# Optimization experiments

Measured on AMD Instinct MI355X. Metric: run time of the kernel, lower is better.

Reference implementation:

```python
import jax, jax.numpy as jnp
import numpy as np

EPS = 1e-12  # F.normalize eps


def _l2norm(v):
    n = jnp.sqrt(jnp.sum(v * v, axis=-1, keepdims=True))
    return v / jnp.maximum(n, EPS)


def setup_inputs() -> dict:
    key = jax.random.key(0)
    ks = jax.random.split(key, 6)
    B, S, D, F, E = 2, 2048, 1024, 4096, 8
    std = 0.02
    return {
        "x": jax.random.normal(ks[0], (B, S, D), jnp.float32),
        "Wp": jax.random.normal(ks[1], (D, D), jnp.float32) * (1.0 / np.sqrt(D)),
        "sim_matrix": jax.random.normal(ks[2], (E, D), jnp.float32) * std,
        "temperature": jnp.asarray(1.0, jnp.float32),
        "W1": jax.random.normal(ks[3], (E, D, F), jnp.float32) * (1.0 / np.sqrt(D)),
        "b1": jnp.zeros((E, F), jnp.float32),
        "W2": jax.random.normal(ks[4], (E, F, D), jnp.float32) * (1.0 / np.sqrt(F)),
        "b2": jnp.zeros((E, D), jnp.float32),
    }


def reference(x, Wp, sim_matrix, temperature, W1, b1, W2, b2):
    # ---- cosine gate ----
    E = sim_matrix.shape[0]
    top_k = 2
    proj = jnp.einsum("bsd,ed->bse", x, Wp)            # Linear(d,d), weight [out,in]
    pn = _l2norm(proj)                                   # [B,S,D]
    sn = _l2norm(sim_matrix)                             # [E,D]
    gate_scores = jnp.einsum("bsd,ed->bse", pn, sn) / temperature
    top_v, top_i = jax.lax.top_k(gate_scores, top_k)     # [B,S,K]
    gate_probs = jax.nn.softmax(top_v, axis=-1)          # [B,S,K]
    # per-token combine weight per expert: sum_k prob_k * 1[idx_k==e]
    comb = jnp.sum(jax.nn.one_hot(top_i, E, dtype=x.dtype) * gate_probs[..., None], axis=-2)  # [B,S,E]
    # ---- experts (dense over all experts, masked combine = original math) ----
    h = jax.nn.gelu(jnp.einsum("bsd,edf->ebsf", x, W1) + b1[:, None, None, :], approximate=False)
    eo = jnp.einsum("ebsf,efd->ebsd", h, W2) + b2[:, None, None, :]  # [E,B,S,D]
    out = jnp.einsum("ebsd,bse->bsd", eo, comb)
    return out
```

## Files before the change

### kernel.cpp

```cpp
#include <hip/hip_runtime.h>
#include <hip/hip_bf16.h>
#include <math.h>

#define NTOK 4096
#define DD 1024
#define FF 4096
#define NEXP 8
#define EBM 128
#define EBN 128
#define EBK 32
#define PAIR_CAP 9216
#define TILES_MAX 72

typedef short bf16x8 __attribute__((ext_vector_type(8)));
typedef float f32x4 __attribute__((ext_vector_type(4)));
typedef unsigned short u16x8 __attribute__((ext_vector_type(8)));

__device__ __forceinline__ ushort f2bf(float x) {
  unsigned u = __float_as_uint(x);
  unsigned r = (u + 0x7FFFu + ((u >> 16) & 1u)) >> 16;
  return (ushort)r;
}

__device__ __forceinline__ void async16(const void* g, void* l) {
  __builtin_amdgcn_global_load_lds(
      (const __attribute__((address_space(1))) char*)g,
      (__attribute__((address_space(3))) char*)l, 16, 0, 0);
}


__global__ void k_convert4(const float4* __restrict__ s, ushort* __restrict__ d, int n4) {
  int i = blockIdx.x * 256 + threadIdx.x;
  if (i >= n4) return;
  float4 v = s[i];
  ushort4 o;
  o.x = f2bf(v.x); o.y = f2bf(v.y); o.z = f2bf(v.z); o.w = f2bf(v.w);
  *(ushort4*)(d + (size_t)i * 4) = o;
}

__global__ void k_transpose(const float* __restrict__ src, ushort* __restrict__ dst,
                            int R, int C) {
  __shared__ float tile[128][65];
  int e = blockIdx.z;
  const float* s = src + (size_t)e * R * C;
  ushort* d = dst + (size_t)e * R * C;
  int c0 = blockIdx.x * 64, r0 = blockIdx.y * 128;
  int tid = threadIdx.x;
  int rr0 = tid >> 4;
  int cc4 = (tid & 15) * 4;
#pragma unroll
  for (int ps = 0; ps < 8; ++ps) {
    int r = ps * 16 + rr0;
    float4 v = *(const float4*)&s[(size_t)(r0 + r) * C + c0 + cc4];
    tile[r][cc4 + 0] = v.x; tile[r][cc4 + 1] = v.y;
    tile[r][cc4 + 2] = v.z; tile[r][cc4 + 3] = v.w;
  }
  __syncthreads();
  int cw = tid >> 4;
  int rp = (tid & 15) * 8;
#pragma unroll
  for (int pass = 0; pass < 4; ++pass) {
    int c = pass * 16 + cw;
    u16x8 o;
#pragma unroll
    for (int k = 0; k < 8; ++k) o[k] = f2bf(tile[rp + k][c]);
    *(u16x8*)&d[(size_t)(c0 + c) * R + r0 + rp] = o;
  }
}

__global__ void k_simnorm(const float* __restrict__ sim, double* __restrict__ snorm) {
  int wid = threadIdx.x >> 6, lane = threadIdx.x & 63;
  double s = 0.0;
  for (int d = lane; d < DD; d += 64) { double v = sim[wid * DD + d]; s += v * v; }
#pragma unroll
  for (int m = 32; m; m >>= 1) s += __shfl_down(s, m);
  if (lane == 0) snorm[wid] = sqrt(s);
}

__global__ void k_u(const float* __restrict__ wp, const float* __restrict__ sim,
                    const double* __restrict__ snorm, double* __restrict__ u) {
  int d = blockIdx.x * 256 + threadIdx.x;
  int e = blockIdx.y;
  double acc = 0.0;
#pragma unroll 8
  for (int o = 0; o < DD; ++o)
    acc += (double)wp[(size_t)o * DD + d] * (double)sim[e * DD + o];
  u[e * DD + d] = acc / fmax(snorm[e], 1e-12);
}

__global__ void k_nured(const float* __restrict__ part, float* __restrict__ nu) {
  int t = blockIdx.x * 256 + threadIdx.x;
  float s = 0.f;
#pragma unroll
  for (int i = 0; i < 16; ++i) s += part[t * 16 + i];
  nu[t] = s;
}

__global__ void k_gate(const float* __restrict__ x, const double* __restrict__ u,
                       const float* __restrict__ nu, const float* __restrict__ temp,
                       int* __restrict__ t2e, float* __restrict__ t2p) {
  int wid = threadIdx.x >> 6, lane = threadIdx.x & 63;
  int t = blockIdx.x * 4 + wid;
  double acc[NEXP];
#pragma unroll
  for (int e = 0; e < NEXP; ++e) acc[e] = 0.0;
  for (int d = lane; d < DD; d += 64) {
    double xv = x[(size_t)t * DD + d];
#pragma unroll
    for (int e = 0; e < NEXP; ++e) acc[e] += xv * u[e * DD + d];
  }
#pragma unroll
  for (int e = 0; e < NEXP; ++e)
    for (int m = 32; m; m >>= 1) acc[e] += __shfl_down(acc[e], m);
  if (lane == 0) {
    double den = fmax(sqrt((double)nu[t]), 1e-12) * (double)temp[0];
    double s[NEXP];
#pragma unroll
    for (int e = 0; e < NEXP; ++e) s[e] = acc[e] / den;
    int e1 = 0; double v1 = s[0];
    for (int e = 1; e < NEXP; ++e) if (s[e] > v1) { v1 = s[e]; e1 = e; }
    int e2 = -1; double v2 = -1e300;
    for (int e = 0; e < NEXP; ++e) if (e != e1 && s[e] > v2) { v2 = s[e]; e2 = e; }
    double z = exp(v2 - v1);
    double inv = 1.0 / (1.0 + z);
    t2e[t * 2] = e1; t2e[t * 2 + 1] = e2;
    t2p[t * 2] = (float)inv; t2p[t * 2 + 1] = (float)(z * inv);
  }
}

__global__ void k_count(const int* __restrict__ t2e, int* __restrict__ meta,
                        int* __restrict__ ptok, float* __restrict__ pp) {
  __shared__ int cnt[NEXP];
  int tid = threadIdx.x;
  if (tid < NEXP) cnt[tid] = 0;
  __syncthreads();
  for (int i = tid; i < NTOK * 2; i += 256) atomicAdd(&cnt[t2e[i]], 1);
  __syncthreads();
  if (tid == 0) {
    int off = 0;
    for (int e = 0; e < NEXP; ++e) {
      meta[e] = cnt[e];
      meta[8 + e] = off;
      off += ((cnt[e] + EBM - 1) / EBM) * EBM;
    }
    meta[16] = off;
    meta[17] = off / EBM;
    for (int e = 0; e < NEXP; ++e) meta[18 + e] = 0;
    int ti = 0;
    for (int e = 0; e < NEXP; ++e) {
      int nt = (cnt[e] + EBM - 1) / EBM;
      for (int k = 0; k < nt; ++k) meta[26 + ti++] = e;
    }
  }
  for (int i = tid; i < PAIR_CAP; i += 256) { ptok[i] = 0; pp[i] = 0.f; }
}

__global__ void k_scatter(const int* __restrict__ t2e, const float* __restrict__ t2p,
                          int* __restrict__ meta, int* __restrict__ ptok,
                          float* __restrict__ pp) {
  int i = blockIdx.x * 256 + threadIdx.x;
  if (i >= NTOK * 2) return;
  int e = t2e[i];
  int slot = atomicAdd(&meta[18 + e], 1);
  int pos = meta[8 + e] + slot;
  ptok[pos] = i >> 1;
  pp[pos] = t2p[i];
}

template <int EPI>
__launch_bounds__(256, 4)
__global__ void gemm_x(const ushort* __restrict__ Abase, const ushort* __restrict__ Bbase,
                       int K, int Brows,
                       const int* __restrict__ pair_tok, const float* __restrict__ pair_p,
                       const int* __restrict__ meta, const float* __restrict__ bias,
                       float* __restrict__ nu_part, ushort* __restrict__ hout,
                       float* __restrict__ outp, int g_tiles, int nby, int tile0) {
  __shared__ ushort As[2][EBM * EBK];
  __shared__ ushort Bs[2][EBN * EBK];
  __shared__ int tok_s[EBM];
  __shared__ float p_s[EBM];

  const int tid = threadIdx.x;
  const int lane = tid & 63;
  const int wid = tid >> 6;

  int tile, nb;
  {
    int bid = blockIdx.x;
    if ((g_tiles & 1) == 0 && (nby & 3) == 0) {
      int x = bid & 7, b = bid >> 3;
      int i = x >> 2, j = x & 3;
      int nt = g_tiles >> 1, np = nby >> 2;
      int t_loc = b / np, p_loc = b - t_loc * np;
      tile = i * nt + t_loc;
      nb = j * np + p_loc;
    } else {
      tile = bid % g_tiles;
      nb = bid / g_tiles;
    }
  }
  tile += tile0;

  int expert = 0;
  if constexpr (EPI != 0) {
    if (tile >= meta[17]) return;
    expert = meta[26 + tile];
    if (tid < EBM) {
      int pr = tile * EBM + tid;
      tok_s[tid] = pair_tok[pr];
      p_s[tid] = pair_p[pr];
    }
    __syncthreads();
  }

  const char* Ac = (const char*)Abase;
  const char* Bc = (const char*)(Bbase + (size_t)expert * Brows * K);

  const char* asrc[2];
  const char* bsrc[2];
#pragma unroll
  for (int i = 0; i < 2; ++i) {
    int c = i * 256 + tid;
    int m = c >> 2, cc = c & 3;
    int sw = (cc ^ (m & 3)) << 4;
    int arow;
    if constexpr (EPI == 1) arow = tok_s[m];
    else if constexpr (EPI == 2) arow = (tile - tile0) * EBM + m;
    else arow = tile * EBM + m;
    asrc[i] = Ac + (size_t)arow * K * 2 + sw;
    bsrc[i] = Bc + (size_t)(nb * EBN + m) * K * 2 + sw;
  }

  const int wr = wid >> 1, wc = wid & 1;
  const int l15 = lane & 15, lg = lane >> 4;

  f32x4 acc[4][4];
#pragma unroll
  for (int a = 0; a < 4; ++a)
#pragma unroll
    for (int b = 0; b < 4; ++b) acc[a][b] = (f32x4){0.f, 0.f, 0.f, 0.f};

  const int nk = K / EBK;

#pragma unroll
  for (int i = 0; i < 2; ++i) {
    async16(asrc[i], (char*)(&As[0][0]) + (i * 256 + wid * 64) * 16);
    async16(bsrc[i], (char*)(&Bs[0][0]) + (i * 256 + wid * 64) * 16);
  }

  for (int kt = 0; kt < nk; ++kt) {
    const int cur = kt & 1;
    __syncthreads();
    if (kt + 1 < nk) {
      const size_t ko = (size_t)(kt + 1) * EBK * 2;
#pragma unroll
      for (int i = 0; i < 2; ++i) {
        async16(asrc[i] + ko, (char*)(&As[cur ^ 1][0]) + (i * 256 + wid * 64) * 16);
        async16(bsrc[i] + ko, (char*)(&Bs[cur ^ 1][0]) + (i * 256 + wid * 64) * 16);
      }
    }
    const char* Ab = (const char*)(&As[cur][0]);
    const char* Bb = (const char*)(&Bs[cur][0]);
    bf16x8 af[4], bfr[4];
#pragma unroll
    for (int fi = 0; fi < 4; ++fi) {
      int r = wr * 64 + fi * 16 + l15;
      int cidx = lg ^ (r & 3);
      af[fi] = *(const bf16x8*)(Ab + r * 64 + cidx * 16);
    }
#pragma unroll
    for (int fj = 0; fj < 4; ++fj) {
      int r = wc * 64 + fj * 16 + l15;
      int cidx = lg ^ (r & 3);
      bfr[fj] = *(const bf16x8*)(Bb + r * 64 + cidx * 16);
    }
#pragma unroll
    for (int fi = 0; fi < 4; ++fi)
#pragma unroll
      for (int fj = 0; fj < 4; ++fj)
        acc[fi][fj] =
            __builtin_amdgcn_mfma_f32_16x16x32_bf16(af[fi], bfr[fj], acc[fi][fj], 0, 0, 0);
  }

  if constexpr (EPI == 0) {
#pragma unroll
    for (int fi = 0; fi < 4; ++fi) {
#pragma unroll
      for (int j = 0; j < 4; ++j) {
        float s = 0.f;
#pragma unroll
        for (int fj = 0; fj < 4; ++fj) { float v = acc[fi][fj][j]; s += v * v; }
        s += __shfl_xor(s, 1); s += __shfl_xor(s, 2);
        s += __shfl_xor(s, 4); s += __shfl_xor(s, 8);
        if (l15 == 0) {
          int row = tile * EBM + wr * 64 + fi * 16 + lg * 4 + j;
          nu_part[row * 16 + nb * 2 + wc] = s;
        }
      }
    }
  } else if constexpr (EPI == 1) {
    float bv[4];
#pragma unroll
    for (int fj = 0; fj < 4; ++fj)
      bv[fj] = bias[expert * FF + nb * EBN + wc * 64 + fj * 16 + l15];
#pragma unroll
    for (int fi = 0; fi < 4; ++fi)
#pragma unroll
      for (int fj = 0; fj < 4; ++fj)
#pragma unroll
        for (int j = 0; j < 4; ++j) {
          float v = acc[fi][fj][j] + bv[fj];
          float g = 0.5f * v * (1.0f + erff(v * 0.70710678118654752f));
          int rl = wr * 64 + fi * 16 + lg * 4 + j;
          size_t grow = (size_t)(tile - tile0) * EBM + rl;
          int col = nb * EBN + wc * 64 + fj * 16 + l15;
          hout[grow * FF + col] = f2bf(g);
        }
  } else {
    float bv[4];
#pragma unroll
    for (int fj = 0; fj < 4; ++fj)
      bv[fj] = bias[expert * DD + nb * EBN + wc * 64 + fj * 16 + l15];
#pragma unroll
    for (int fi = 0; fi < 4; ++fi) {
      int rl = wr * 64 + fi * 16 + lg * 4;
#pragma unroll
      for (int j = 0; j < 4; ++j) {
        int tok = tok_s[rl + j];
        float p = p_s[rl + j];
#pragma unroll
        for (int fj = 0; fj < 4; ++fj) {
          float v = (acc[fi][fj][j] + bv[fj]) * p;
          int col = nb * EBN + wc * 64 + fj * 16 + l15;
          atomicAdd(outp + (size_t)tok * DD + col, v);
        }
      }
    }
  }
}


extern "C" void kernel_launch(void* const* d_in, const int* in_sizes, int n_in,
                              void* d_out, int out_size, void* d_ws, size_t ws_size,
                              hipStream_t stream) {
  const float* x = (const float*)d_in[0];
  const float* wp = (const float*)d_in[1];
  const float* sim = (const float*)d_in[2];
  const float* temp = (const float*)d_in[3];
  const float* w1 = (const float*)d_in[4];
  const float* b1 = (const float*)d_in[5];
  const float* w2 = (const float*)d_in[6];
  const float* b2 = (const float*)d_in[7];
  float* out = (float*)d_out;

  char* w = (char*)d_ws;
  size_t off = 0;
  auto alloc = [&](size_t sz) {
    char* p = w + off;
    off = (off + sz + 255) & ~(size_t)255;
    return p;
  };
  double* u = (double*)alloc((size_t)NEXP * DD * 8);
  double* snorm = (double*)alloc(NEXP * 8);
  float* nu_part = (float*)alloc((size_t)NTOK * 16 * 4);
  float* nu = (float*)alloc((size_t)NTOK * 4);
  int* t2e = (int*)alloc((size_t)NTOK * 2 * 4);
  float* t2p = (float*)alloc((size_t)NTOK * 2 * 4);
  int* meta = (int*)alloc(512);
  int* ptok = (int*)alloc((size_t)PAIR_CAP * 4);
  float* pp = (float*)alloc((size_t)PAIR_CAP * 4);
  ushort* xbf = (ushort*)alloc((size_t)NTOK * DD * 2);
  ushort* wpbf = (ushort*)alloc((size_t)DD * DD * 2);
  ushort* w1t = (ushort*)alloc((size_t)NEXP * DD * FF * 2);
  ushort* w2t = (ushort*)alloc((size_t)NEXP * DD * FF * 2);
  size_t havail = (ws_size > off) ? (ws_size - off) : 0;
  int G = (int)(havail / ((size_t)EBM * FF * 2));
  if (G > TILES_MAX) G = TILES_MAX;
  if (G >= 8) G &= ~7;
  if (G < 1) G = 1;
  ushort* h = (ushort*)(w + off);

  hipMemsetAsync(d_out, 0, (size_t)out_size * 4, stream);

  k_convert4<<<dim3(NTOK * DD / 4 / 256), 256, 0, stream>>>((const float4*)x, xbf, NTOK * DD / 4);
  k_convert4<<<dim3(DD * DD / 4 / 256), 256, 0, stream>>>((const float4*)wp, wpbf, DD * DD / 4);
  k_transpose<<<dim3(FF / 64, DD / 128, NEXP), 256, 0, stream>>>(w1, w1t, DD, FF);
  k_transpose<<<dim3(DD / 64, FF / 128, NEXP), 256, 0, stream>>>(w2, w2t, FF, DD);
  k_simnorm<<<1, 512, 0, stream>>>(sim, snorm);
  k_u<<<dim3(DD / 256, NEXP), 256, 0, stream>>>(wp, sim, snorm, u);
  gemm_x<0><<<dim3((NTOK / EBM) * (DD / EBN)), 256, 0, stream>>>(
      xbf, wpbf, DD, DD, nullptr, nullptr, nullptr, nullptr, nu_part, nullptr, nullptr,
      NTOK / EBM, DD / EBN, 0);
  k_nured<<<dim3(NTOK / 256), 256, 0, stream>>>(nu_part, nu);
  k_gate<<<dim3(NTOK / 4), 256, 0, stream>>>(x, u, nu, temp, t2e, t2p);
  k_count<<<1, 256, 0, stream>>>(t2e, meta, ptok, pp);
  k_scatter<<<dim3(NTOK * 2 / 256), 256, 0, stream>>>(t2e, t2p, meta, ptok, pp);

  for (int t0 = 0; t0 < TILES_MAX; t0 += G) {
    int g = TILES_MAX - t0;
    if (g > G) g = G;
    gemm_x<1><<<dim3(g * (FF / EBN)), 256, 0, stream>>>(
        xbf, w1t, DD, FF, ptok, pp, meta, b1, nullptr, h, nullptr, g, FF / EBN, t0);
    gemm_x<2><<<dim3(g * (DD / EBN)), 256, 0, stream>>>(
        h, w2t, FF, DD, ptok, pp, meta, b2, nullptr, nullptr, out, g, DD / EBN, t0);
  }
}
```

Baseline: 545.8 us.

## Fuse small gating kernels, split u reduction, tweak LDS swizzle and occupancy

Merges sim-norm into k_u and splits its K loop four ways with a separate reduction kernel. k_nured is folded into k_gate and k_scatter into k_count, which removes launches. In gemm_x the token/prob shared-memory staging and its barrier are replaced by direct global loads. The LDS swizzle changes to XOR on (row>>1)&3, and launch bounds rise to 5 waves per SIMD. This trades fewer launches and syncs against more register pressure, a single-block scatter, and repeated global reads in the epilogue.

```diff
diff --git a/kernel.cpp b/kernel.cpp
--- a/kernel.cpp
+++ b/kernel.cpp
@@ -68,36 +68,40 @@
   }
 }
 
-__global__ void k_simnorm(const float* __restrict__ sim, double* __restrict__ snorm) {
-  int wid = threadIdx.x >> 6, lane = threadIdx.x & 63;
+__global__ void k_u(const float* __restrict__ wp, const float* __restrict__ sim,
+                    double* __restrict__ u_part) {
+  __shared__ double sred[256];
+  int tid = threadIdx.x;
+  int dblk = blockIdx.x, e = blockIdx.y, kc = blockIdx.z;
   double s = 0.0;
-  for (int d = lane; d < DD; d += 64) { double v = sim[wid * DD + d]; s += v * v; }
-#pragma unroll
-  for (int m = 32; m; m >>= 1) s += __shfl_down(s, m);
-  if (lane == 0) snorm[wid] = sqrt(s);
-}
-
-__global__ void k_u(const float* __restrict__ wp, const float* __restrict__ sim,
-                    const double* __restrict__ snorm, double* __restrict__ u) {
-  int d = blockIdx.x * 256 + threadIdx.x;
-  int e = blockIdx.y;
+#pragma unroll
+  for (int j = 0; j < 4; ++j) {
+    double v = sim[e * DD + j * 256 + tid];
+    s += v * v;
+  }
+  sred[tid] = s;
+  __syncthreads();
+  for (int m = 128; m; m >>= 1) {
+    if (tid < m) sred[tid] += sred[tid + m];
+    __syncthreads();
+  }
+  double sn = fmax(sqrt(sred[0]), 1e-12);
+  int d = dblk * 256 + tid;
+  int o0 = kc * 256;
   double acc = 0.0;
 #pragma unroll 8
-  for (int o = 0; o < DD; ++o)
+  for (int o = o0; o < o0 + 256; ++o)
     acc += (double)wp[(size_t)o * DD + d] * (double)sim[e * DD + o];
-  u[e * DD + d] = acc / fmax(snorm[e], 1e-12);
-}
-
-__global__ void k_nured(const float* __restrict__ part, float* __restrict__ nu) {
-  int t = blockIdx.x * 256 + threadIdx.x;
-  float s = 0.f;
-#pragma unroll
-  for (int i = 0; i < 16; ++i) s += part[t * 16 + i];
-  nu[t] = s;
+  u_part[((size_t)kc * NEXP + e) * DD + d] = acc / sn;
+}
+
+__global__ void k_ured(const double* __restrict__ up, double* __restrict__ u) {
+  int i = blockIdx.x * 256 + threadIdx.x;
+  u[i] = (up[i] + up[8192 + i]) + (up[16384 + i] + up[24576 + i]);
 }
 
 __global__ void k_gate(const float* __restrict__ x, const double* __restrict__ u,
-                       const float* __restrict__ nu, const float* __restrict__ temp,
+                       const float* __restrict__ nu_part, const float* __restrict__ temp,
                        int* __restrict__ t2e, float* __restrict__ t2p) {
   int wid = threadIdx.x >> 6, lane = threadIdx.x & 63;
   int t = blockIdx.x * 4 + wid;
@@ -112,8 +116,11 @@
 #pragma unroll
   for (int e = 0; e < NEXP; ++e)
     for (int m = 32; m; m >>= 1) acc[e] += __shfl_down(acc[e], m);
+  float nv = (lane < 16) ? nu_part[t * 16 + lane] : 0.f;
+  nv += __shfl_down(nv, 8); nv += __shfl_down(nv, 4);
+  nv += __shfl_down(nv, 2); nv += __shfl_down(nv, 1);
   if (lane == 0) {
-    double den = fmax(sqrt((double)nu[t]), 1e-12) * (double)temp[0];
+    double den = fmax(sqrt((double)nv), 1e-12) * (double)temp[0];
     double s[NEXP];
 #pragma unroll
     for (int e = 0; e < NEXP; ++e) s[e] = acc[e] / den;
@@ -128,10 +135,12 @@
   }
 }
 
-__global__ void k_count(const int* __restrict__ t2e, int* __restrict__ meta,
-                        int* __restrict__ ptok, float* __restrict__ pp) {
+__global__ void k_count(const int* __restrict__ t2e, const float* __restrict__ t2p,
+                        int* __restrict__ meta, int* __restrict__ ptok,
+                        float* __restrict__ pp) {
   __shared__ int cnt[NEXP];
   int tid = threadIdx.x;
+  for (int i = tid; i < PAIR_CAP; i += 256) { ptok[i] = 0; pp[i] = 0.f; }
   if (tid < NEXP) cnt[tid] = 0;
   __syncthreads();
   for (int i = tid; i < NTOK * 2; i += 256) atomicAdd(&cnt[t2e[i]], 1);
@@ -152,23 +161,18 @@
       for (int k = 0; k < nt; ++k) meta[26 + ti++] = e;
     }
   }
-  for (int i = tid; i < PAIR_CAP; i += 256) { ptok[i] = 0; pp[i] = 0.f; }
-}
-
-__global__ void k_scatter(const int* __restrict__ t2e, const float* __restrict__ t2p,
-                          int* __restrict__ meta, int* __restrict__ ptok,
-                          float* __restrict__ pp) {
-  int i = blockIdx.x * 256 + threadIdx.x;
-  if (i >= NTOK * 2) return;
-  int e = t2e[i];
-  int slot = atomicAdd(&meta[18 + e], 1);
-  int pos = meta[8 + e] + slot;
-  ptok[pos] = i >> 1;
-  pp[pos] = t2p[i];
+  __syncthreads();
+  for (int i = tid; i < NTOK * 2; i += 256) {
+    int e = t2e[i];
+    int slot = atomicAdd(&meta[18 + e], 1);
+    int pos = meta[8 + e] + slot;
+    ptok[pos] = i >> 1;
+    pp[pos] = t2p[i];
+  }
 }
 
 template <int EPI>
-__launch_bounds__(256, 4)
+__launch_bounds__(256, 5)
 __global__ void gemm_x(const ushort* __restrict__ Abase, const ushort* __restrict__ Bbase,
                        int K, int Brows,
                        const int* __restrict__ pair_tok, const float* __restrict__ pair_p,
@@ -177,8 +181,6 @@
                        float* __restrict__ outp, int g_tiles, int nby, int tile0) {
   __shared__ ushort As[2][EBM * EBK];
   __shared__ ushort Bs[2][EBN * EBK];
-  __shared__ int tok_s[EBM];
-  __shared__ float p_s[EBM];
 
   const int tid = threadIdx.x;
   const int lane = tid & 63;
@@ -205,12 +207,6 @@
   if constexpr (EPI != 0) {
     if (tile >= meta[17]) return;
     expert = meta[26 + tile];
-    if (tid < EBM) {
-      int pr = tile * EBM + tid;
-      tok_s[tid] = pair_tok[pr];
-      p_s[tid] = pair_p[pr];
-    }
-    __syncthreads();
   }
 
   const char* Ac = (const char*)Abase;
@@ -222,9 +218,9 @@
   for (int i = 0; i < 2; ++i) {
     int c = i * 256 + tid;
     int m = c >> 2, cc = c & 3;
-    int sw = (cc ^ (m & 3)) << 4;
+    int sw = (cc ^ ((m >> 1) & 3)) << 4;
     int arow;
-    if constexpr (EPI == 1) arow = tok_s[m];
+    if constexpr (EPI == 1) arow = pair_tok[tile * EBM + m];
     else if constexpr (EPI == 2) arow = (tile - tile0) * EBM + m;
     else arow = tile * EBM + m;
     asrc[i] = Ac + (size_t)arow * K * 2 + sw;
@@ -233,6 +229,7 @@
 
   const int wr = wid >> 1, wc = wid & 1;
   const int l15 = lane & 15, lg = lane >> 4;
+  const int fxor = (l15 >> 1) & 3;
 
   f32x4 acc[4][4];
 #pragma unroll
@@ -265,14 +262,12 @@
 #pragma unroll
     for (int fi = 0; fi < 4; ++fi) {
       int r = wr * 64 + fi * 16 + l15;
-      int cidx = lg ^ (r & 3);
-      af[fi] = *(const bf16x8*)(Ab + r * 64 + cidx * 16);
+      af[fi] = *(const bf16x8*)(Ab + r * 64 + (lg ^ fxor) * 16);
     }
 #pragma unroll
     for (int fj = 0; fj < 4; ++fj) {
       int r = wc * 64 + fj * 16 + l15;
-      int cidx = lg ^ (r & 3);
-      bfr[fj] = *(const bf16x8*)(Bb + r * 64 + cidx * 16);
+      bfr[fj] = *(const bf16x8*)(Bb + r * 64 + (lg ^ fxor) * 16);
     }
 #pragma unroll
     for (int fi = 0; fi < 4; ++fi)
@@ -321,13 +316,14 @@
 #pragma unroll
     for (int fj = 0; fj < 4; ++fj)
       bv[fj] = bias[expert * DD + nb * EBN + wc * 64 + fj * 16 + l15];
+    const int prb = tile * EBM;
 #pragma unroll
     for (int fi = 0; fi < 4; ++fi) {
       int rl = wr * 64 + fi * 16 + lg * 4;
 #pragma unroll
       for (int j = 0; j < 4; ++j) {
-        int tok = tok_s[rl + j];
-        float p = p_s[rl + j];
+        int tok = pair_tok[prb + rl + j];
+        float p = pair_p[prb + rl + j];
 #pragma unroll
         for (int fj = 0; fj < 4; ++fj) {
           float v = (acc[fi][fj][j] + bv[fj]) * p;
@@ -361,9 +357,8 @@
     return p;
   };
   double* u = (double*)alloc((size_t)NEXP * DD * 8);
-  double* snorm = (double*)alloc(NEXP * 8);
+  double* u_part = (double*)alloc((size_t)4 * NEXP * DD * 8);
   float* nu_part = (float*)alloc((size_t)NTOK * 16 * 4);
-  float* nu = (float*)alloc((size_t)NTOK * 4);
   int* t2e = (int*)alloc((size_t)NTOK * 2 * 4);
   float* t2p = (float*)alloc((size_t)NTOK * 2 * 4);
   int* meta = (int*)alloc(512);
@@ -386,15 +381,13 @@
   k_convert4<<<dim3(DD * DD / 4 / 256), 256, 0, stream>>>((const float4*)wp, wpbf, DD * DD / 4);
   k_transpose<<<dim3(FF / 64, DD / 128, NEXP), 256, 0, stream>>>(w1, w1t, DD, FF);
   k_transpose<<<dim3(DD / 64, FF / 128, NEXP), 256, 0, stream>>>(w2, w2t, FF, DD);
-  k_simnorm<<<1, 512, 0, stream>>>(sim, snorm);
-  k_u<<<dim3(DD / 256, NEXP), 256, 0, stream>>>(wp, sim, snorm, u);
+  k_u<<<dim3(DD / 256, NEXP, 4), 256, 0, stream>>>(wp, sim, u_part);
+  k_ured<<<dim3(NEXP * DD / 256), 256, 0, stream>>>(u_part, u);
   gemm_x<0><<<dim3((NTOK / EBM) * (DD / EBN)), 256, 0, stream>>>(
       xbf, wpbf, DD, DD, nullptr, nullptr, nullptr, nullptr, nu_part, nullptr, nullptr,
       NTOK / EBM, DD / EBN, 0);
-  k_nured<<<dim3(NTOK / 256), 256, 0, stream>>>(nu_part, nu);
-  k_gate<<<dim3(NTOK / 4), 256, 0, stream>>>(x, u, nu, temp, t2e, t2p);
-  k_count<<<1, 256, 0, stream>>>(t2e, meta, ptok, pp);
-  k_scatter<<<dim3(NTOK * 2 / 256), 256, 0, stream>>>(t2e, t2p, meta, ptok, pp);
+  k_gate<<<dim3(NTOK / 4), 256, 0, stream>>>(x, u, nu_part, temp, t2e, t2p);
+  k_count<<<1, 256, 0, stream>>>(t2e, t2p, meta, ptok, pp);
 
   for (int t0 = 0; t0 < TILES_MAX; t0 += G) {
     int g = TILES_MAX - t0;
```

Result: slower. 601.2 us (+10.2%).
